# Performance work log

Measured on AMD Instinct MI355X. Metric: run time of the kernel, lower is better.

The kernel has to match this reference:

```python
import jax, jax.numpy as jnp
import numpy as np

N_HEADS = 16

def setup_inputs() -> dict:
    key = jax.random.key(0)
    k1, k2 = jax.random.split(key)
    qkv = jax.random.normal(k1, (4, 3072, 2048), dtype=jnp.float32)
    encoder_kv = jax.random.normal(k2, (4, 2048, 256), dtype=jnp.float32)
    return {"qkv": qkv, "encoder_kv": encoder_kv}

def reference(qkv, encoder_kv):
    bs, width, length = qkv.shape
    ch = width // (3 * N_HEADS)  # 64
    # [bs*H, 3*ch, T] -> q, k, v each [bs*H, ch, T]
    q, k, v = jnp.split(qkv.reshape(bs * N_HEADS, 3 * ch, length), 3, axis=1)
    # encoder kv: [bs, H*2*ch, S] -> ek, ev each [bs*H, ch, S]
    ek, ev = jnp.split(encoder_kv.reshape(bs * N_HEADS, 2 * ch, -1), 2, axis=1)
    k = jnp.concatenate([ek, k], axis=-1)  # [bs*H, ch, S+T]
    v = jnp.concatenate([ev, v], axis=-1)
    scale = ch ** -0.25  # 1/sqrt(sqrt(ch)), applied to both q and k
    weight = jnp.einsum('bct,bcs->bts', q * scale, k * scale)  # [bs*H, T, S+T]
    weight = jax.nn.softmax(weight.astype(jnp.float32), axis=-1).astype(qkv.dtype)
    a = jnp.einsum('bts,bcs->bct', weight, v)  # [bs*H, ch, T]
    return a.reshape(bs, -1, length)
```

## Files before the change

kernel.cpp:

```cpp
#include <hip/hip_runtime.h>
#include <hip/hip_bf16.h>

typedef __attribute__((ext_vector_type(8))) short bf16x8;
typedef __attribute__((ext_vector_type(8))) short s16x8;
typedef __attribute__((ext_vector_type(4))) short s16x4;
typedef __attribute__((ext_vector_type(4))) float f32x4;

#define T_LEN 2048
#define S_ENC 256
#define ROW 72
#define QSCALE 0.18033688011112042f

#if __has_builtin(__builtin_amdgcn_exp2f)
#define EXP2(x) __builtin_amdgcn_exp2f(x)
#else
#define EXP2(x) exp2f(x)
#endif

__device__ __forceinline__ short f2bf(float x) {
  union { __hip_bfloat16 b; short s; } u;
  u.b = __float2bfloat16(x);
  return u.s;
}

template<int STRIDE>
__device__ __forceinline__ void tile_body(
    const float* __restrict__ kb, const float* __restrict__ vb, int s0,
    short* __restrict__ Kt, short* __restrict__ Vt,
    const bf16x8 (&qf)[2][2], f32x4 (&o)[2][4], float (&lp)[2], int tid) {

  const int lane = tid & 63;
  const int ln = lane & 15;
  const int lg = lane >> 4;

  const int ks = tid & 63;
  const int kc = (tid >> 6) * 8;
  float kr[8];
  const float* kp = kb + (size_t)kc * STRIDE + (s0 + ks);
#pragma unroll
  for (int r = 0; r < 8; ++r) kr[r] = kp[(size_t)r * STRIDE];

  const int vg = tid & 15;
  const int vc = tid >> 4;
  const int vcol = 32 * (vg >> 3) + 8 * (vg & 3) + 4 * ((vg >> 2) & 1);
  const float* vp0 = vb + (size_t)vc * STRIDE + (s0 + 4 * vg);
  f32x4 vr0 = *(const f32x4*)(vp0);
  f32x4 vr1 = *(const f32x4*)(vp0 + (size_t)32 * STRIDE);

  __syncthreads();

  s16x8 kw;
#pragma unroll
  for (int r = 0; r < 8; ++r) kw[r] = f2bf(kr[r]);
  *(s16x8*)(Kt + ks * ROW + kc) = kw;

  s16x4 vw;
#pragma unroll
  for (int i = 0; i < 4; ++i) vw[i] = f2bf(vr0[i]);
  *(s16x4*)(Vt + vc * ROW + vcol) = vw;
#pragma unroll
  for (int i = 0; i < 4; ++i) vw[i] = f2bf(vr1[i]);
  *(s16x4*)(Vt + (vc + 32) * ROW + vcol) = vw;

  __syncthreads();

  f32x4 sacc[2][4];
#pragma unroll
  for (int qt = 0; qt < 2; ++qt)
#pragma unroll
    for (int mt = 0; mt < 4; ++mt) sacc[qt][mt] = (f32x4){0.f, 0.f, 0.f, 0.f};

#pragma unroll
  for (int mt = 0; mt < 4; ++mt) {
    const short* krow = Kt + (16 * mt + ln) * ROW + 8 * lg;
    const bf16x8 kf0 = *(const bf16x8*)(krow);
    const bf16x8 kf1 = *(const bf16x8*)(krow + 32);
#pragma unroll
    for (int qt = 0; qt < 2; ++qt) {
      sacc[qt][mt] = __builtin_amdgcn_mfma_f32_16x16x32_bf16(kf0, qf[qt][0], sacc[qt][mt], 0, 0, 0);
      sacc[qt][mt] = __builtin_amdgcn_mfma_f32_16x16x32_bf16(kf1, qf[qt][1], sacc[qt][mt], 0, 0, 0);
    }
  }

  bf16x8 pfrag[2][2];
#pragma unroll
  for (int qt = 0; qt < 2; ++qt) {
    float ls = 0.f;
#pragma unroll
    for (int mt = 0; mt < 4; ++mt)
#pragma unroll
      for (int r = 0; r < 4; ++r) {
        const float p = EXP2(sacc[qt][mt][r]);
        ls += p;
        pfrag[qt][mt >> 1][4 * (mt & 1) + r] = f2bf(p);
      }
    lp[qt] += ls;
  }

#pragma unroll
  for (int sub = 0; sub < 2; ++sub)
#pragma unroll
    for (int ct = 0; ct < 4; ++ct) {
      const bf16x8 vf = *(const bf16x8*)(Vt + (16 * ct + ln) * ROW + 32 * sub + 8 * lg);
#pragma unroll
      for (int qt = 0; qt < 2; ++qt)
        o[qt][ct] = __builtin_amdgcn_mfma_f32_16x16x32_bf16(vf, pfrag[qt][sub], o[qt][ct], 0, 0, 0);
    }
}

__global__ __launch_bounds__(512, 4) void attn_kernel(
    const float* __restrict__ qkv, const float* __restrict__ ekv,
    float* __restrict__ out) {
  const int tid = threadIdx.x;
  const int lane = tid & 63;
  const int wave = tid >> 6;
  const int ln = lane & 15;
  const int lg = lane >> 4;

  const int bh = blockIdx.x >> 3;
  const int qb = blockIdx.x & 7;
  const int t0 = qb * 256 + wave * 32;

  const float* qp  = qkv + (size_t)bh * 192 * T_LEN;
  const float* kp  = qp + (size_t)64 * T_LEN;
  const float* vp  = qp + (size_t)128 * T_LEN;
  const float* ekp = ekv + (size_t)bh * 128 * S_ENC;
  const float* evp = ekp + (size_t)64 * S_ENC;

  __shared__ __attribute__((aligned(16))) short Kt[64 * ROW];
  __shared__ __attribute__((aligned(16))) short Vt[64 * ROW];

  bf16x8 qf[2][2];
#pragma unroll
  for (int qt = 0; qt < 2; ++qt)
#pragma unroll
    for (int kk = 0; kk < 2; ++kk)
#pragma unroll
      for (int j = 0; j < 8; ++j)
        qf[qt][kk][j] =
            f2bf(qp[(size_t)(32 * kk + 8 * lg + j) * T_LEN + (t0 + 16 * qt + ln)] * QSCALE);

  f32x4 o[2][4];
#pragma unroll
  for (int qt = 0; qt < 2; ++qt)
#pragma unroll
    for (int ct = 0; ct < 4; ++ct) o[qt][ct] = (f32x4){0.f, 0.f, 0.f, 0.f};
  float lp[2] = {0.f, 0.f};

  for (int st = 0; st < 4; ++st)
    tile_body<S_ENC>(ekp, evp, 64 * st, Kt, Vt, qf, o, lp, tid);
  for (int st = 0; st < 32; ++st)
    tile_body<T_LEN>(kp, vp, 64 * st, Kt, Vt, qf, o, lp, tid);

#pragma unroll
  for (int qt = 0; qt < 2; ++qt) {
    float l = lp[qt];
    l += __shfl_xor(l, 16);
    l += __shfl_xor(l, 32);
    const float inv = 1.0f / l;
    float* ob = out + (size_t)bh * 64 * T_LEN + (t0 + 16 * qt + ln);
#pragma unroll
    for (int ct = 0; ct < 4; ++ct)
#pragma unroll
      for (int r = 0; r < 4; ++r)
        ob[(size_t)(16 * ct + 4 * lg + r) * T_LEN] = o[qt][ct][r] * inv;
  }
}

extern "C" void kernel_launch(void* const* d_in, const int* in_sizes, int n_in,
                              void* d_out, int out_size, void* d_ws, size_t ws_size,
                              hipStream_t stream) {
  const float* qkv = (const float*)d_in[0];
  const float* ekv = (const float*)d_in[1];
  float* out = (float*)d_out;
  attn_kernel<<<dim3(512), dim3(512), 0, stream>>>(qkv, ekv, out);
}
```

Baseline: 109.2 us.

## Double-buffer K/V tiles in LDS with register prefetch two tiles ahead

Splits the tile body into load, stage-write and compute phases. K/V tiles are now double-buffered in shared memory, and global loads are issued two tiles ahead, so each iteration needs one barrier instead of two and load latency overlaps the MFMA work. The change also remaps blockIdx so consecutive blocks take different heads, swaps the exp2 builtin for exp2f, and reassociates the row-sum reduction. In exchange, shared memory per block doubles, register pressure rises, and the runtime tile-source select adds branching.

```diff
diff --git a/kernel.cpp b/kernel.cpp
--- a/kernel.cpp
+++ b/kernel.cpp
@@ -8,14 +8,11 @@
 
 #define T_LEN 2048
 #define S_ENC 256
+#define NT 36
 #define ROW 72
 #define QSCALE 0.18033688011112042f
 
-#if __has_builtin(__builtin_amdgcn_exp2f)
-#define EXP2(x) __builtin_amdgcn_exp2f(x)
-#else
 #define EXP2(x) exp2f(x)
-#endif
 
 __device__ __forceinline__ short f2bf(float x) {
   union { __hip_bfloat16 b; short s; } u;
@@ -23,37 +20,43 @@
   return u.s;
 }
 
-template<int STRIDE>
-__device__ __forceinline__ void tile_body(
-    const float* __restrict__ kb, const float* __restrict__ vb, int s0,
-    short* __restrict__ Kt, short* __restrict__ Vt,
-    const bf16x8 (&qf)[2][2], f32x4 (&o)[2][4], float (&lp)[2], int tid) {
-
-  const int lane = tid & 63;
-  const int ln = lane & 15;
-  const int lg = lane >> 4;
-
+struct TileSrc { const float* k; const float* v; int stride; int s0; };
+
+__device__ __forceinline__ TileSrc tsrc(int t, const float* kp, const float* vp,
+                                        const float* ekp, const float* evp) {
+  TileSrc s;
+  if (t < 4) { s.k = ekp; s.v = evp; s.stride = S_ENC; s.s0 = 64 * t; }
+  else       { s.k = kp;  s.v = vp;  s.stride = T_LEN; s.s0 = 64 * (t - 4); }
+  return s;
+}
+
+__device__ __forceinline__ void issue_loads(const TileSrc& s, int tid,
+                                            float (&kr)[8], f32x4& vr0, f32x4& vr1) {
   const int ks = tid & 63;
   const int kc = (tid >> 6) * 8;
-  float kr[8];
-  const float* kp = kb + (size_t)kc * STRIDE + (s0 + ks);
-#pragma unroll
-  for (int r = 0; r < 8; ++r) kr[r] = kp[(size_t)r * STRIDE];
+  const float* kp = s.k + (size_t)kc * s.stride + (s.s0 + ks);
+#pragma unroll
+  for (int r = 0; r < 8; ++r) kr[r] = kp[(size_t)r * s.stride];
+  const int vg = tid & 15;
+  const int vc = tid >> 4;
+  const float* vp0 = s.v + (size_t)vc * s.stride + (s.s0 + 4 * vg);
+  vr0 = *(const f32x4*)(vp0);
+  vr1 = *(const f32x4*)(vp0 + (size_t)32 * s.stride);
+}
+
+__device__ __forceinline__ void stage_write(short* __restrict__ Kt, short* __restrict__ Vt,
+                                            int tid, const float (&kr)[8],
+                                            const f32x4& vr0, const f32x4& vr1) {
+  const int ks = tid & 63;
+  const int kc = (tid >> 6) * 8;
+  s16x8 kw;
+#pragma unroll
+  for (int r = 0; r < 8; ++r) kw[r] = f2bf(kr[r]);
+  *(s16x8*)(Kt + ks * ROW + kc) = kw;
 
   const int vg = tid & 15;
   const int vc = tid >> 4;
   const int vcol = 32 * (vg >> 3) + 8 * (vg & 3) + 4 * ((vg >> 2) & 1);
-  const float* vp0 = vb + (size_t)vc * STRIDE + (s0 + 4 * vg);
-  f32x4 vr0 = *(const f32x4*)(vp0);
-  f32x4 vr1 = *(const f32x4*)(vp0 + (size_t)32 * STRIDE);
-
-  __syncthreads();
-
-  s16x8 kw;
-#pragma unroll
-  for (int r = 0; r < 8; ++r) kw[r] = f2bf(kr[r]);
-  *(s16x8*)(Kt + ks * ROW + kc) = kw;
-
   s16x4 vw;
 #pragma unroll
   for (int i = 0; i < 4; ++i) vw[i] = f2bf(vr0[i]);
@@ -61,9 +64,13 @@
 #pragma unroll
   for (int i = 0; i < 4; ++i) vw[i] = f2bf(vr1[i]);
   *(s16x4*)(Vt + (vc + 32) * ROW + vcol) = vw;
-
-  __syncthreads();
-
+}
+
+__device__ __forceinline__ void compute_tile(const short* __restrict__ Kt,
+                                             const short* __restrict__ Vt,
+                                             const bf16x8 (&qf)[2][2],
+                                             f32x4 (&o)[2][4], float (&lp)[2],
+                                             int ln, int lg) {
   f32x4 sacc[2][4];
 #pragma unroll
   for (int qt = 0; qt < 2; ++qt)
@@ -85,16 +92,20 @@
   bf16x8 pfrag[2][2];
 #pragma unroll
   for (int qt = 0; qt < 2; ++qt) {
-    float ls = 0.f;
-#pragma unroll
-    for (int mt = 0; mt < 4; ++mt)
-#pragma unroll
-      for (int r = 0; r < 4; ++r) {
-        const float p = EXP2(sacc[qt][mt][r]);
-        ls += p;
-        pfrag[qt][mt >> 1][4 * (mt & 1) + r] = f2bf(p);
-      }
-    lp[qt] += ls;
+    float pmt[4];
+#pragma unroll
+    for (int mt = 0; mt < 4; ++mt) {
+      float p0 = EXP2(sacc[qt][mt][0]);
+      float p1 = EXP2(sacc[qt][mt][1]);
+      float p2 = EXP2(sacc[qt][mt][2]);
+      float p3 = EXP2(sacc[qt][mt][3]);
+      pfrag[qt][mt >> 1][4 * (mt & 1) + 0] = f2bf(p0);
+      pfrag[qt][mt >> 1][4 * (mt & 1) + 1] = f2bf(p1);
+      pfrag[qt][mt >> 1][4 * (mt & 1) + 2] = f2bf(p2);
+      pfrag[qt][mt >> 1][4 * (mt & 1) + 3] = f2bf(p3);
+      pmt[mt] = (p0 + p1) + (p2 + p3);
+    }
+    lp[qt] += (pmt[0] + pmt[1]) + (pmt[2] + pmt[3]);
   }
 
 #pragma unroll
@@ -117,8 +128,8 @@
   const int ln = lane & 15;
   const int lg = lane >> 4;
 
-  const int bh = blockIdx.x >> 3;
-  const int qb = blockIdx.x & 7;
+  const int bh = blockIdx.x & 63;
+  const int qb = blockIdx.x >> 6;
   const int t0 = qb * 256 + wave * 32;
 
   const float* qp  = qkv + (size_t)bh * 192 * T_LEN;
@@ -127,8 +138,8 @@
   const float* ekp = ekv + (size_t)bh * 128 * S_ENC;
   const float* evp = ekp + (size_t)64 * S_ENC;
 
-  __shared__ __attribute__((aligned(16))) short Kt[64 * ROW];
-  __shared__ __attribute__((aligned(16))) short Vt[64 * ROW];
+  __shared__ __attribute__((aligned(16))) short Kt[2][64 * ROW];
+  __shared__ __attribute__((aligned(16))) short Vt[2][64 * ROW];
 
   bf16x8 qf[2][2];
 #pragma unroll
@@ -147,10 +158,24 @@
     for (int ct = 0; ct < 4; ++ct) o[qt][ct] = (f32x4){0.f, 0.f, 0.f, 0.f};
   float lp[2] = {0.f, 0.f};
 
-  for (int st = 0; st < 4; ++st)
-    tile_body<S_ENC>(ekp, evp, 64 * st, Kt, Vt, qf, o, lp, tid);
-  for (int st = 0; st < 32; ++st)
-    tile_body<T_LEN>(kp, vp, 64 * st, Kt, Vt, qf, o, lp, tid);
+  float kr[8];
+  f32x4 vr0, vr1;
+  issue_loads(tsrc(0, kp, vp, ekp, evp), tid, kr, vr0, vr1);
+  stage_write(&Kt[0][0], &Vt[0][0], tid, kr, vr0, vr1);
+  issue_loads(tsrc(1, kp, vp, ekp, evp), tid, kr, vr0, vr1);
+  __syncthreads();
+
+  int cur = 0;
+  for (int t = 0; t < NT; ++t) {
+    if (t + 1 < NT) {
+      stage_write(&Kt[cur ^ 1][0], &Vt[cur ^ 1][0], tid, kr, vr0, vr1);
+      if (t + 2 < NT)
+        issue_loads(tsrc(t + 2, kp, vp, ekp, evp), tid, kr, vr0, vr1);
+    }
+    compute_tile(&Kt[cur][0], &Vt[cur][0], qf, o, lp, ln, lg);
+    __syncthreads();
+    cur ^= 1;
+  }
 
 #pragma unroll
   for (int qt = 0; qt < 2; ++qt) {
```

Result: slower. 136.3 us (+24.8%).
